# Kernel optimization log

Hardware: AMD Instinct MI355X
Metric: run time of the kernel (lower is better)

Reference implementation:

```python
import jax, jax.numpy as jnp
import numpy as np

N, H, W, D, K = 32, 36, 36, 512, 64
POOL = 3  # pool_list=[3] -> 3x3 grid of regions
EPS = 1e-12


def setup_inputs() -> dict:
    key = jax.random.key(0)
    k1, k2, k3 = jax.random.split(key, 3)
    x = jax.random.normal(k1, (N, H, W, D), dtype=jnp.float32)
    W_conv = jax.random.normal(k2, (D, K), dtype=jnp.float32) * 0.05
    C = jax.random.normal(k3, (D, K), dtype=jnp.float32) * 0.05
    return {"x": x, "W_conv": W_conv, "C": C}


def _l2norm(v, axis):
    return v / jnp.sqrt(jnp.sum(v * v, axis=axis, keepdims=True) + EPS)


def _encode_vlad(xm, W_conv, C):
    # xm: [N, h, w, D]
    s = jnp.einsum('nhwd,dk->nhwk', xm, W_conv)          # 1x1 conv, no bias
    a = jax.nn.softmax(s, axis=-1)                        # soft assignment [N,h,w,K]
    # Faithful to sum_hw a * (x[...,None] - C) without the [N,h,w,D,K] blow-up:
    # = einsum(x, a) - C * sum_hw(a)
    asum = jnp.sum(a, axis=(1, 2))                        # [N, K]
    v = jnp.einsum('nhwd,nhwk->ndk', xm, a) - C[None] * asum[:, None, :]  # [N, D, K]
    # intra-normalization: normalize each cluster's residual over D
    v = _l2norm(v, axis=1)                                # [N, D, K]
    v = v.reshape(v.shape[0], -1)                         # flatten (row-major, matches tf)
    v = _l2norm(v, axis=-1)                               # [N, D*K]
    return v


def reference(x, W_conv, C):
    n, h, w, d = x.shape
    rl, cl = h / POOL, w / POOL
    outs = []
    for jy in range(POOL):
        for ix in range(POOL):
            y1, y2 = int(round(jy * rl)), int(round(jy * rl + rl))
            x1, x2 = int(round(ix * cl)), int(round(ix * cl + cl))
            outs.append(_encode_vlad(x[:, y1:y2, x1:x2, :], W_conv, C))
    return jnp.concatenate(outs, axis=1)  # [N, POOL*POOL*D*K]
```

## Files before the change

kernel.cpp:

```cpp
#include <hip/hip_runtime.h>

typedef __attribute__((ext_vector_type(4))) float f32x4;
typedef __attribute__((ext_vector_type(8))) short short8;

#define EPSF 1e-12f

__device__ __forceinline__ ushort bf16rne(float x) {
  uint u = __float_as_uint(x);
  u += 0x7fffu + ((u >> 16) & 1u);
  return (ushort)(u >> 16);
}
__device__ __forceinline__ float bf2f(ushort h) {
  return __uint_as_float(((uint)h) << 16);
}
__device__ __forceinline__ f32x4 mfma16(short8 a, short8 b, f32x4 c) {
  return __builtin_amdgcn_mfma_f32_16x16x32_bf16(a, b, c, 0, 0, 0);
}
__device__ __forceinline__ short8 frag64(const ushort* base, int row, int kofs) {
  int g = kofs >> 3;
  int sg = g ^ (row & 7);
  return *(const short8*)(base + row * 64 + (sg << 3));
}

__global__ __launch_bounds__(256) void k0_wt(const float* __restrict__ W,
                                             ushort* __restrict__ wsWT) {
  int k = blockIdx.x;
  for (int d = threadIdx.x; d < 512; d += 256) {
    float v = W[(size_t)d * 64 + k];
    ushort h = bf16rne(v);
    wsWT[k * 512 + d] = h;
    wsWT[32768 + k * 512 + d] = bf16rne(v - bf2f(h));
  }
}

__global__ __launch_bounds__(256, 5) void k1_assign(
    const float* __restrict__ x, const ushort* __restrict__ wsWT,
    float4* __restrict__ aT_ws, float* __restrict__ asum_ws) {
  __shared__ char sm[30208];
  ushort* xsH = (ushort*)(sm);
  ushort* xsL = (ushort*)(sm + 6144);
  ushort* wtH = (ushort*)(sm + 12288);
  ushort* wtL = (ushort*)(sm + 20480);
  float* smax = (float*)(sm + 28672);
  float* ssum = (float*)(sm + 29440);
  ushort* atH = (ushort*)(sm);
  ushort* atL = (ushort*)(sm + 7168);

  int b = blockIdx.x;
  int region = b / 3, third = b % 3;
  int n = region / 9, r = region % 9;
  int y1 = (r / 3) * 12, x1 = (r % 3) * 12;
  int p0 = third * 48;
  int t = threadIdx.x;
  int w = t >> 6;
  int lane = t & 63, l15 = lane & 15, hi16 = lane >> 4;
  const float* xn = x + (size_t)n * (36 * 36 * 512);

  float4 px[2][2];
  short8 pwH[2], pwL[2];
  int ntask = (t < 128) ? 2 : 1;

  f32x4 acc[3];
#pragma unroll
  for (int ni = 0; ni < 3; ++ni) acc[ni] = (f32x4){0.f, 0.f, 0.f, 0.f};

  {
#pragma unroll
    for (int i = 0; i < 2; ++i)
      if (i < ntask) {
        int task = t + i * 256;
        int p = task >> 3, g = task & 7;
        int pr = p0 + p;
        const float* src = xn + ((size_t)(y1 + pr / 12) * 36 + (x1 + pr % 12)) * 512 + g * 8;
        px[i][0] = *(const float4*)src;
        px[i][1] = *(const float4*)(src + 4);
      }
#pragma unroll
    for (int i = 0; i < 2; ++i) {
      int task = t + i * 256;
      int wk = task >> 3, wg = task & 7;
      pwH[i] = *(const short8*)(wsWT + wk * 512 + wg * 8);
      pwL[i] = *(const short8*)(wsWT + 32768 + wk * 512 + wg * 8);
    }
  }

  for (int c = 0; c < 8; ++c) {
    __syncthreads();
#pragma unroll
    for (int i = 0; i < 2; ++i)
      if (i < ntask) {
        int task = t + i * 256;
        int p = task >> 3, g = task & 7;
        float vals[8] = {px[i][0].x, px[i][0].y, px[i][0].z, px[i][0].w,
                         px[i][1].x, px[i][1].y, px[i][1].z, px[i][1].w};
        short8 h8, l8;
#pragma unroll
        for (int j = 0; j < 8; ++j) {
          ushort h = bf16rne(vals[j]);
          h8[j] = (short)h;
          l8[j] = (short)bf16rne(vals[j] - bf2f(h));
        }
        int sg = g ^ (p & 7);
        *(short8*)(xsH + p * 64 + (sg << 3)) = h8;
        *(short8*)(xsL + p * 64 + (sg << 3)) = l8;
      }
#pragma unroll
    for (int i = 0; i < 2; ++i) {
      int task = t + i * 256;
      int wk = task >> 3, wg = task & 7;
      int sg = wg ^ (wk & 7);
      *(short8*)(wtH + wk * 64 + (sg << 3)) = pwH[i];
      *(short8*)(wtL + wk * 64 + (sg << 3)) = pwL[i];
    }
    if (c < 7) {
      int d0 = (c + 1) * 64;
#pragma unroll
      for (int i = 0; i < 2; ++i)
        if (i < ntask) {
          int task = t + i * 256;
          int p = task >> 3, g = task & 7;
          int pr = p0 + p;
          const float* src = xn + ((size_t)(y1 + pr / 12) * 36 + (x1 + pr % 12)) * 512 + d0 + g * 8;
          px[i][0] = *(const float4*)src;
          px[i][1] = *(const float4*)(src + 4);
        }
#pragma unroll
      for (int i = 0; i < 2; ++i) {
        int task = t + i * 256;
        int wk = task >> 3, wg = task & 7;
        pwH[i] = *(const short8*)(wsWT + wk * 512 + d0 + wg * 8);
        pwL[i] = *(const short8*)(wsWT + 32768 + wk * 512 + d0 + wg * 8);
      }
    }
    __syncthreads();

#pragma unroll
    for (int ks = 0; ks < 2; ++ks) {
      int kofs = ks * 32 + hi16 * 8;
      short8 aH = frag64(wtH, w * 16 + l15, kofs);
      short8 aL = frag64(wtL, w * 16 + l15, kofs);
#pragma unroll
      for (int ni = 0; ni < 3; ++ni) {
        short8 bH = frag64(xsH, ni * 16 + l15, kofs);
        short8 bL = frag64(xsL, ni * 16 + l15, kofs);
        f32x4 a0 = acc[ni];
        a0 = mfma16(aH, bH, a0);
        a0 = mfma16(aH, bL, a0);
        a0 = mfma16(aL, bH, a0);
        acc[ni] = a0;
      }
    }
  }
  __syncthreads();

  float lm[3];
#pragma unroll
  for (int ni = 0; ni < 3; ++ni) {
    float m = fmaxf(fmaxf(acc[ni][0], acc[ni][1]), fmaxf(acc[ni][2], acc[ni][3]));
    m = fmaxf(m, __shfl_xor(m, 16));
    m = fmaxf(m, __shfl_xor(m, 32));
    lm[ni] = m;
  }
  if (hi16 == 0)
#pragma unroll
    for (int ni = 0; ni < 3; ++ni) smax[w * 48 + ni * 16 + l15] = lm[ni];
  __syncthreads();

  float e[3][4], ls[3];
#pragma unroll
  for (int ni = 0; ni < 3; ++ni) {
    int p = ni * 16 + l15;
    float M = fmaxf(fmaxf(smax[0 * 48 + p], smax[1 * 48 + p]),
                    fmaxf(smax[2 * 48 + p], smax[3 * 48 + p]));
    float s = 0.f;
#pragma unroll
    for (int rr = 0; rr < 4; ++rr) {
      e[ni][rr] = __expf(acc[ni][rr] - M);
      s += e[ni][rr];
    }
    s += __shfl_xor(s, 16);
    s += __shfl_xor(s, 32);
    ls[ni] = s;
  }
  if (hi16 == 0)
#pragma unroll
    for (int ni = 0; ni < 3; ++ni) ssum[w * 48 + ni * 16 + l15] = ls[ni];
  __syncthreads();

  float part[4];
#pragma unroll
  for (int rr = 0; rr < 4; ++rr) part[rr] = 0.f;

#pragma unroll
  for (int ni = 0; ni < 3; ++ni) {
    int p = ni * 16 + l15;
    float S = ssum[0 * 48 + p] + ssum[1 * 48 + p] + ssum[2 * 48 + p] + ssum[3 * 48 + p];
    float inv = 1.f / S;
#pragma unroll
    for (int rr = 0; rr < 4; ++rr) {
      float a = e[ni][rr] * inv;
      part[rr] += a;
      int k = w * 16 + hi16 * 4 + rr;
      ushort h = bf16rne(a);
      atH[k * 56 + p] = h;
      atL[k * 56 + p] = bf16rne(a - bf2f(h));
    }
  }
#pragma unroll
  for (int rr = 0; rr < 4; ++rr) {
    float s = part[rr];
    s += __shfl_xor(s, 1);
    s += __shfl_xor(s, 2);
    s += __shfl_xor(s, 4);
    s += __shfl_xor(s, 8);
    if (l15 == 0) asum_ws[b * 64 + w * 16 + hi16 * 4 + rr] = s;
  }
  __syncthreads();

  {
    float4* dst = aT_ws + (size_t)region * 2432;
    for (int i = t; i < 768; i += 256) {
      int plane = i / 384;
      int rem = i - plane * 384;
      int row = rem / 6, c4 = rem - row * 6;
      float4 v = *(const float4*)(sm + plane * 7168 + row * 112 + c4 * 16);
      dst[plane * 1216 + row * 19 + third * 6 + c4] = v;
    }
    if (third == 2) {
      float4 z = {0.f, 0.f, 0.f, 0.f};
      for (int i = t; i < 128; i += 256) {
        int plane = i >> 6, row = i & 63;
        dst[plane * 1216 + row * 19 + 18] = z;
      }
    }
  }
}

__global__ __launch_bounds__(512, 8) void k2_vlad(
    const float* __restrict__ x, const float* __restrict__ C,
    const float4* __restrict__ aT_ws, const float* __restrict__ asum_ws,
    float* __restrict__ out, float* __restrict__ colnorm) {
  __shared__ float4 smv[2504];
  char* sm = (char*)smv;
  ushort* atH = (ushort*)sm;
  ushort* atL = (ushort*)(sm + 19456);
  int* poff = (int*)(sm + 38912);
  float* asumS = (float*)(sm + 39552);
  float* cn2 = (float*)(sm + 39808);

  int b = blockIdx.x;
  int reg = b % 288;
  int dc = b / 288;
  int n = reg / 9, r = reg % 9;
  int d0 = dc * 64;
  int y1 = (r / 3) * 12, x1 = (r % 3) * 12;
  int t = threadIdx.x;
  int w = t >> 6, lane = t & 63, l15 = lane & 15, hi16 = lane >> 4;
  const float* xn = x + (size_t)n * (36 * 36 * 512);

  if (t < 160) poff[t] = (t < 144) ? ((y1 + t / 12) * 36 + (x1 + t % 12)) * 512 : 0;
  if (t < 64) {
    asumS[t] = asum_ws[(reg * 3) * 64 + t] + asum_ws[(reg * 3 + 1) * 64 + t] +
               asum_ws[(reg * 3 + 2) * 64 + t];
    cn2[t] = 0.f;
  }
  {
    const float4* src = aT_ws + (size_t)reg * 2432;
    for (int i = t; i < 2432; i += 512) smv[i] = src[i];
  }
  __syncthreads();

  int mi = w & 3, kh = w >> 2;
  int drow = d0 + mi * 16 + l15;
  const float* xcol = xn + drow;

  f32x4 acc[2];
  acc[0] = (f32x4){0.f, 0.f, 0.f, 0.f};
  acc[1] = (f32x4){0.f, 0.f, 0.f, 0.f};

#pragma unroll
  for (int ks = 0; ks < 5; ++ks) {
    int pb = ks * 32 + hi16 * 8;
    int4 poA = *reinterpret_cast<const int4*>(&poff[pb]);
    int4 poB = *reinterpret_cast<const int4*>(&poff[pb + 4]);
    float av[8];
    av[0] = xcol[poA.x]; av[1] = xcol[poA.y];
    av[2] = xcol[poA.z]; av[3] = xcol[poA.w];
    av[4] = xcol[poB.x]; av[5] = xcol[poB.y];
    av[6] = xcol[poB.z]; av[7] = xcol[poB.w];
    bool valid = (ks < 4) || (hi16 < 2);
    short8 ah, al;
#pragma unroll
    for (int j = 0; j < 8; ++j) {
      float v = valid ? av[j] : 0.f;
      ushort h = bf16rne(v);
      ah[j] = (short)h;
      al[j] = (short)bf16rne(v - bf2f(h));
    }
#pragma unroll
    for (int ni = 0; ni < 2; ++ni) {
      int row = kh * 32 + ni * 16 + l15;
      short8 bh = *(const short8*)(atH + row * 152 + pb);
      short8 bl = *(const short8*)(atL + row * 152 + pb);
      f32x4 a0 = acc[ni];
      a0 = mfma16(ah, bh, a0);
      a0 = mfma16(ah, bl, a0);
      a0 = mfma16(al, bh, a0);
      acc[ni] = a0;
    }
  }

  size_t obase = (size_t)reg * (512 * 64);
#pragma unroll
  for (int ni = 0; ni < 2; ++ni) {
    int k = kh * 32 + ni * 16 + l15;
    float ak = asumS[k];
    float s2 = 0.f;
#pragma unroll
    for (int rr = 0; rr < 4; ++rr) {
      int d = d0 + mi * 16 + hi16 * 4 + rr;
      float v = acc[ni][rr] - C[(size_t)d * 64 + k] * ak;
      out[obase + (size_t)d * 64 + k] = v;
      s2 += v * v;
    }
    atomicAdd(&cn2[k], s2);
  }
  __syncthreads();
  if (t < 64) colnorm[(size_t)(reg * 8 + dc) * 64 + t] = cn2[t];
}

__global__ __launch_bounds__(256) void k3_scale(float* __restrict__ out,
                                                const float* __restrict__ colnorm) {
  int b = blockIdx.x;
  int reg = b % 288;
  int dc = b / 288;

  __shared__ float ratio[64];
  __shared__ float fs[64];
  int t = threadIdx.x;
  float c = 0.f;
  if (t < 64) {
#pragma unroll
    for (int j = 0; j < 8; ++j) c += colnorm[(size_t)(reg * 8 + j) * 64 + t];
    ratio[t] = c / (c + EPSF);
  }
  __syncthreads();
  if (t < 64) {
    float g = 0.f;
#pragma unroll
    for (int j = 0; j < 64; ++j) g += ratio[j];
    fs[t] = rsqrtf(c + EPSF) * rsqrtf(g + EPSF);
  }
  __syncthreads();

  size_t base4 = (((size_t)reg * 512) + (size_t)dc * 128) * 64 / 4;
  float4* o4 = reinterpret_cast<float4*>(out);
  for (int j = 0; j < 8; ++j) {
    size_t idx = base4 + t + 256 * j;
    float4 v = o4[idx];
    int k0 = (int)((idx * 4) & 63);
    v.x *= fs[k0]; v.y *= fs[k0 + 1]; v.z *= fs[k0 + 2]; v.w *= fs[k0 + 3];
    o4[idx] = v;
  }
}

extern "C" void kernel_launch(void* const* d_in, const int* in_sizes, int n_in,
                              void* d_out, int out_size, void* d_ws, size_t ws_size,
                              hipStream_t stream) {
  const float* x = (const float*)d_in[0];
  const float* Wc = (const float*)d_in[1];
  const float* C = (const float*)d_in[2];
  float* out = (float*)d_out;

  char* ws = (char*)d_ws;
  ushort* wsWT = (ushort*)(ws);
  float* asum_ws = (float*)(ws + 131072);
  float* colnorm = (float*)(ws + 352256);
  float4* aT_ws = (float4*)(ws + 942080);

  k0_wt<<<64, 256, 0, stream>>>(Wc, wsWT);
  k1_assign<<<864, 256, 0, stream>>>(x, wsWT, aT_ws, asum_ws);
  k2_vlad<<<2304, 512, 0, stream>>>(x, C, aT_ws, asum_ws, out, colnorm);
  k3_scale<<<1152, 256, 0, stream>>>(out, colnorm);
}
```

Measured before the change: 78.37 us.

## Load MFMA fragments directly from global memory and use packed bf16 conversion

The k1_assign GEMM stops staging x and W tiles through swizzled shared memory with double-buffered registers and barriers. Each lane now loads its MFMA fragments straight from global memory, and the loop over D is fully unrolled. Float-to-bf16 hi/lo splitting moves to the hardware v_cvt_pk_bf16_f32 instruction, replacing manual round-to-nearest-even bit manipulation, and this also applies in the second kernel. The launch-bounds occupancy hint drops from 5 to 4 and shared memory shrinks. The cost is less coalesced, redundant global/L2 reads: each wave reloads x rows and each x fragment is fetched by all four waves.

```diff
diff --git a/kernel.cpp b/kernel.cpp
--- a/kernel.cpp
+++ b/kernel.cpp
@@ -13,13 +13,31 @@
 __device__ __forceinline__ float bf2f(ushort h) {
   return __uint_as_float(((uint)h) << 16);
 }
+__device__ __forceinline__ uint cvtpk(float lo, float hi) {
+  uint r;
+  asm("v_cvt_pk_bf16_f32 %0, %1, %2" : "=v"(r) : "v"(lo), "v"(hi));
+  return r;
+}
+union US8 { uint4 u; short8 s; };
+__device__ __forceinline__ void cvt8hl(float4 v0, float4 v1, short8& h8, short8& l8) {
+  US8 h, l;
+  h.u.x = cvtpk(v0.x, v0.y);
+  h.u.y = cvtpk(v0.z, v0.w);
+  h.u.z = cvtpk(v1.x, v1.y);
+  h.u.w = cvtpk(v1.z, v1.w);
+  float r0 = __uint_as_float(h.u.x << 16), r1 = __uint_as_float(h.u.x & 0xffff0000u);
+  float r2 = __uint_as_float(h.u.y << 16), r3 = __uint_as_float(h.u.y & 0xffff0000u);
+  float r4 = __uint_as_float(h.u.z << 16), r5 = __uint_as_float(h.u.z & 0xffff0000u);
+  float r6 = __uint_as_float(h.u.w << 16), r7 = __uint_as_float(h.u.w & 0xffff0000u);
+  l.u.x = cvtpk(v0.x - r0, v0.y - r1);
+  l.u.y = cvtpk(v0.z - r2, v0.w - r3);
+  l.u.z = cvtpk(v1.x - r4, v1.y - r5);
+  l.u.w = cvtpk(v1.z - r6, v1.w - r7);
+  h8 = h.s;
+  l8 = l.s;
+}
 __device__ __forceinline__ f32x4 mfma16(short8 a, short8 b, f32x4 c) {
   return __builtin_amdgcn_mfma_f32_16x16x32_bf16(a, b, c, 0, 0, 0);
-}
-__device__ __forceinline__ short8 frag64(const ushort* base, int row, int kofs) {
-  int g = kofs >> 3;
-  int sg = g ^ (row & 7);
-  return *(const short8*)(base + row * 64 + (sg << 3));
 }
 
 __global__ __launch_bounds__(256) void k0_wt(const float* __restrict__ W,
@@ -33,18 +51,14 @@
   }
 }
 
-__global__ __launch_bounds__(256, 5) void k1_assign(
+__global__ __launch_bounds__(256, 4) void k1_assign(
     const float* __restrict__ x, const ushort* __restrict__ wsWT,
     float4* __restrict__ aT_ws, float* __restrict__ asum_ws) {
-  __shared__ char sm[30208];
-  ushort* xsH = (ushort*)(sm);
-  ushort* xsL = (ushort*)(sm + 6144);
-  ushort* wtH = (ushort*)(sm + 12288);
-  ushort* wtL = (ushort*)(sm + 20480);
-  float* smax = (float*)(sm + 28672);
-  float* ssum = (float*)(sm + 29440);
-  ushort* atH = (ushort*)(sm);
+  __shared__ char sm[15872];
+  ushort* atH = (ushort*)sm;
   ushort* atL = (ushort*)(sm + 7168);
+  float* smax = (float*)(sm + 14336);
+  float* ssum = (float*)(sm + 15104);
 
   int b = blockIdx.x;
   int region = b / 3, third = b % 3;
@@ -56,102 +70,66 @@
   int lane = t & 63, l15 = lane & 15, hi16 = lane >> 4;
   const float* xn = x + (size_t)n * (36 * 36 * 512);
 
-  float4 px[2][2];
-  short8 pwH[2], pwL[2];
-  int ntask = (t < 128) ? 2 : 1;
+  const float* pb0;
+  const float* pb1;
+  const float* pb2;
+  {
+    int pr0 = p0 + 0 * 16 + l15;
+    int pr1 = p0 + 1 * 16 + l15;
+    int pr2 = p0 + 2 * 16 + l15;
+    pb0 = xn + ((size_t)(y1 + pr0 / 12) * 36 + (x1 + pr0 % 12)) * 512 + hi16 * 8;
+    pb1 = xn + ((size_t)(y1 + pr1 / 12) * 36 + (x1 + pr1 % 12)) * 512 + hi16 * 8;
+    pb2 = xn + ((size_t)(y1 + pr2 / 12) * 36 + (x1 + pr2 % 12)) * 512 + hi16 * 8;
+  }
+  const ushort* aBaseH = wsWT + (w * 16 + l15) * 512 + hi16 * 8;
+  const ushort* aBaseL = aBaseH + 32768;
 
   f32x4 acc[3];
 #pragma unroll
   for (int ni = 0; ni < 3; ++ni) acc[ni] = (f32x4){0.f, 0.f, 0.f, 0.f};
 
-  {
-#pragma unroll
-    for (int i = 0; i < 2; ++i)
-      if (i < ntask) {
-        int task = t + i * 256;
-        int p = task >> 3, g = task & 7;
-        int pr = p0 + p;
-        const float* src = xn + ((size_t)(y1 + pr / 12) * 36 + (x1 + pr % 12)) * 512 + g * 8;
-        px[i][0] = *(const float4*)src;
-        px[i][1] = *(const float4*)(src + 4);
-      }
-#pragma unroll
-    for (int i = 0; i < 2; ++i) {
-      int task = t + i * 256;
-      int wk = task >> 3, wg = task & 7;
-      pwH[i] = *(const short8*)(wsWT + wk * 512 + wg * 8);
-      pwL[i] = *(const short8*)(wsWT + 32768 + wk * 512 + wg * 8);
-    }
-  }
-
+#pragma unroll
   for (int c = 0; c < 8; ++c) {
-    __syncthreads();
-#pragma unroll
-    for (int i = 0; i < 2; ++i)
-      if (i < ntask) {
-        int task = t + i * 256;
-        int p = task >> 3, g = task & 7;
-        float vals[8] = {px[i][0].x, px[i][0].y, px[i][0].z, px[i][0].w,
-                         px[i][1].x, px[i][1].y, px[i][1].z, px[i][1].w};
-        short8 h8, l8;
-#pragma unroll
-        for (int j = 0; j < 8; ++j) {
-          ushort h = bf16rne(vals[j]);
-          h8[j] = (short)h;
-          l8[j] = (short)bf16rne(vals[j] - bf2f(h));
-        }
-        int sg = g ^ (p & 7);
-        *(short8*)(xsH + p * 64 + (sg << 3)) = h8;
-        *(short8*)(xsL + p * 64 + (sg << 3)) = l8;
-      }
-#pragma unroll
-    for (int i = 0; i < 2; ++i) {
-      int task = t + i * 256;
-      int wk = task >> 3, wg = task & 7;
-      int sg = wg ^ (wk & 7);
-      *(short8*)(wtH + wk * 64 + (sg << 3)) = pwH[i];
-      *(short8*)(wtL + wk * 64 + (sg << 3)) = pwL[i];
-    }
-    if (c < 7) {
-      int d0 = (c + 1) * 64;
-#pragma unroll
-      for (int i = 0; i < 2; ++i)
-        if (i < ntask) {
-          int task = t + i * 256;
-          int p = task >> 3, g = task & 7;
-          int pr = p0 + p;
-          const float* src = xn + ((size_t)(y1 + pr / 12) * 36 + (x1 + pr % 12)) * 512 + d0 + g * 8;
-          px[i][0] = *(const float4*)src;
-          px[i][1] = *(const float4*)(src + 4);
-        }
-#pragma unroll
-      for (int i = 0; i < 2; ++i) {
-        int task = t + i * 256;
-        int wk = task >> 3, wg = task & 7;
-        pwH[i] = *(const short8*)(wsWT + wk * 512 + d0 + wg * 8);
-        pwL[i] = *(const short8*)(wsWT + 32768 + wk * 512 + d0 + wg * 8);
-      }
-    }
-    __syncthreads();
-
 #pragma unroll
     for (int ks = 0; ks < 2; ++ks) {
-      int kofs = ks * 32 + hi16 * 8;
-      short8 aH = frag64(wtH, w * 16 + l15, kofs);
-      short8 aL = frag64(wtL, w * 16 + l15, kofs);
-#pragma unroll
-      for (int ni = 0; ni < 3; ++ni) {
-        short8 bH = frag64(xsH, ni * 16 + l15, kofs);
-        short8 bL = frag64(xsL, ni * 16 + l15, kofs);
-        f32x4 a0 = acc[ni];
+      const int off = c * 64 + ks * 32;
+      short8 aH = *(const short8*)(aBaseH + off);
+      short8 aL = *(const short8*)(aBaseL + off);
+      {
+        float4 v0 = *(const float4*)(pb0 + off);
+        float4 v1 = *(const float4*)(pb0 + off + 4);
+        short8 bH, bL;
+        cvt8hl(v0, v1, bH, bL);
+        f32x4 a0 = acc[0];
         a0 = mfma16(aH, bH, a0);
         a0 = mfma16(aH, bL, a0);
         a0 = mfma16(aL, bH, a0);
-        acc[ni] = a0;
+        acc[0] = a0;
       }
-    }
-  }
-  __syncthreads();
+      {
+        float4 v0 = *(const float4*)(pb1 + off);
+        float4 v1 = *(const float4*)(pb1 + off + 4);
+        short8 bH, bL;
+        cvt8hl(v0, v1, bH, bL);
+        f32x4 a0 = acc[1];
+        a0 = mfma16(aH, bH, a0);
+        a0 = mfma16(aH, bL, a0);
+        a0 = mfma16(aL, bH, a0);
+        acc[1] = a0;
+      }
+      {
+        float4 v0 = *(const float4*)(pb2 + off);
+        float4 v1 = *(const float4*)(pb2 + off + 4);
+        short8 bH, bL;
+        cvt8hl(v0, v1, bH, bL);
+        f32x4 a0 = acc[2];
+        a0 = mfma16(aH, bH, a0);
+        a0 = mfma16(aH, bL, a0);
+        a0 = mfma16(aL, bH, a0);
+        acc[2] = a0;
+      }
+    }
+  }
 
   float lm[3];
 #pragma unroll
@@ -283,20 +261,18 @@
     int pb = ks * 32 + hi16 * 8;
     int4 poA = *reinterpret_cast<const int4*>(&poff[pb]);
     int4 poB = *reinterpret_cast<const int4*>(&poff[pb + 4]);
-    float av[8];
-    av[0] = xcol[poA.x]; av[1] = xcol[poA.y];
-    av[2] = xcol[poA.z]; av[3] = xcol[poA.w];
-    av[4] = xcol[poB.x]; av[5] = xcol[poB.y];
-    av[6] = xcol[poB.z]; av[7] = xcol[poB.w];
     bool valid = (ks < 4) || (hi16 < 2);
+    float4 u0, u1;
+    u0.x = valid ? xcol[poA.x] : 0.f;
+    u0.y = valid ? xcol[poA.y] : 0.f;
+    u0.z = valid ? xcol[poA.z] : 0.f;
+    u0.w = valid ? xcol[poA.w] : 0.f;
+    u1.x = valid ? xcol[poB.x] : 0.f;
+    u1.y = valid ? xcol[poB.y] : 0.f;
+    u1.z = valid ? xcol[poB.z] : 0.f;
+    u1.w = valid ? xcol[poB.w] : 0.f;
     short8 ah, al;
-#pragma unroll
-    for (int j = 0; j < 8; ++j) {
-      float v = valid ? av[j] : 0.f;
-      ushort h = bf16rne(v);
-      ah[j] = (short)h;
-      al[j] = (short)bf16rne(v - bf2f(h));
-    }
+    cvt8hl(u0, u1, ah, al);
 #pragma unroll
     for (int ni = 0; ni < 2; ++ni) {
       int row = kh * 32 + ni * 16 + l15;
```

New measurement: 116.6 us. 1.49x slower.
